# Kernel tuning notes

Hardware: AMD Instinct MI355X
Metric: run time of the kernel (lower is better)

Reference implementation:

```python
import jax, jax.numpy as jnp
import numpy as np

B, T, E, H, V = 64, 512, 512, 1024, 32000


def setup_inputs() -> dict:
    key = jax.random.key(0)
    k1, k2, k3, k4, k5 = jax.random.split(key, 5)
    scale = 1.0 / np.sqrt(H)
    return {
        "source": jax.random.randint(k1, (B, T), 0, V),
        "emb_table": jax.random.normal(k2, (V, E), dtype=jnp.float32),
        "W_ih": jax.random.normal(k3, (E, 4 * H), dtype=jnp.float32) * scale,
        "W_hh": jax.random.normal(k4, (H, 4 * H), dtype=jnp.float32) * scale,
        "b": jax.random.normal(k5, (4 * H,), dtype=jnp.float32) * scale,
    }


def reference(source, emb_table, W_ih, W_hh, b):
    # Embedding lookup: [B, T, E]
    embedded = emb_table[source]
    batch = source.shape[0]
    hidden = W_hh.shape[0]
    h0 = jnp.zeros((batch, hidden), dtype=emb_table.dtype)
    c0 = jnp.zeros((batch, hidden), dtype=emb_table.dtype)

    # Sequential LSTM cell loop over timesteps, expressed as lax.scan.
    xs = jnp.swapaxes(embedded, 0, 1)  # [T, B, E]

    def step(carry, x_t):
        h, c = carry
        z = x_t @ W_ih + h @ W_hh + b  # [B, 4H]
        i, f, g, o = jnp.split(z, 4, axis=-1)
        i = jax.nn.sigmoid(i)
        f = jax.nn.sigmoid(f)
        g = jnp.tanh(g)
        o = jax.nn.sigmoid(o)
        c_new = f * c + i * g
        h_new = o * jnp.tanh(c_new)
        return (h_new, c_new), None

    (h_T, c_T), _ = jax.lax.scan(step, (h0, c0), xs)
    return h_T, c_T
```

## Files before the change

### kernel.cpp

```cpp
#include <hip/hip_runtime.h>
#include <hip/hip_bf16.h>

#define TT 512
#define BB 64
#define EE 512
#define HH 1024

typedef __attribute__((ext_vector_type(8))) short short8;
typedef __attribute__((ext_vector_type(4))) float f32x4;
typedef __attribute__((ext_vector_type(4))) unsigned int u32x4;

#define WS_X     0
#define WS_WT    33554432
#define WS_HBUF  46137344
#define WS_PROBE 48496640

#define POISON 0x7F7F7F7Fu

static __device__ __forceinline__ unsigned short f2bf(float x) {
    unsigned int u = __float_as_uint(x);
    unsigned int r = (u + 0x7fffu + ((u >> 16) & 1u)) >> 16;
    return (unsigned short)r;
}

__global__ void embed_k(const int* __restrict__ src, const float* __restrict__ emb,
                        unsigned short* __restrict__ X) {
    int idx  = blockIdx.x * 256 + threadIdx.x;
    int base = idx * 4;
    int t = base >> 15;
    int r = base & 32767;
    int b = r >> 9;
    int e = r & 511;
    int v = src[b * TT + t];
    float4 f = *(const float4*)(emb + (size_t)v * EE + e);
    ushort4 s;
    s.x = f2bf(f.x); s.y = f2bf(f.y); s.z = f2bf(f.z); s.w = f2bf(f.w);
    *(ushort4*)(X + base) = s;
}

__global__ void wprep_k(const float* __restrict__ Wih, const float* __restrict__ Whh,
                        unsigned short* __restrict__ Wt, int* __restrict__ probe) {
    const int bid = blockIdx.x;
    const int kk  = bid % 48;
    const int ct  = bid / 48;
    const int tid = threadIdx.x;

    if (bid == 0 && tid == 0) {
        int xcd;
        asm volatile("s_getreg_b32 %0, hwreg(HW_REG_XCC_ID)" : "=s"(xcd));
        int* pr = probe;
        asm volatile("global_store_dword %0, %1, off sc0"
                     :: "v"(pr), "v"(xcd) : "memory");
        int v;
        asm volatile("global_load_dword %0, %1, off sc0\n\ts_waitcnt vmcnt(0)"
                     : "=v"(v) : "v"(pr) : "memory");
        pr[1] = v;
    }

    const int k0 = kk * 32, c0 = ct * 16;
    __shared__ float tile[32][17];
    for (int e = tid; e < 512; e += 256) {
        int kr = e >> 4, cc = e & 15;
        int k = k0 + kr;
        float v = (k < EE) ? Wih[(size_t)k * 4096 + c0 + cc]
                           : Whh[(size_t)(k - EE) * 4096 + c0 + cc];
        tile[kr][cc] = v;
    }
    __syncthreads();
    for (int e = tid; e < 512; e += 256) {
        int lane = e >> 3, j = e & 7;
        float v = tile[(lane >> 4) * 8 + j][lane & 15];
        Wt[(size_t)bid * 512 + e] = f2bf(v);
    }
}

__global__ __launch_bounds__(256, 1) void lstm_k(
    const unsigned short* __restrict__ X,
    const unsigned short* __restrict__ Wt,
    const float* __restrict__ bias,
    unsigned short* __restrict__ hbuf,
    float* __restrict__ out)
{
    const int g        = blockIdx.x;
    const int cg       = g & 63;
    const int rg       = g >> 6;
    const int row_base = rg * 16;
    const int ubase    = cg * 16;
    const int tid  = threadIdx.x;
    const int wave = tid >> 6;
    const int lane = tid & 63;
    const int lrow = lane & 15;
    const int quad = lane >> 4;
    const int erow = tid >> 4, eu = tid & 15;

    __shared__ float zred[2][4][4][16][17];

    const float bi_ = bias[          ubase + eu];
    const float bf_ = bias[HH      + ubase + eu];
    const float bg_ = bias[2 * HH  + ubase + eu];
    const float bo_ = bias[3 * HH  + ubase + eu];

    short8 wr[12][4];
#pragma unroll
    for (int i = 0; i < 12; ++i) {
        const int kk = i * 4 + wave;
#pragma unroll
        for (int g4 = 0; g4 < 4; ++g4) {
            const int ct = g4 * 64 + cg;
            wr[i][g4] = *(const short8*)(Wt + ((size_t)(ct * 48 + kk)) * 512 + lane * 8);
        }
    }

    float creg = 0.f;

    for (int t = 0; t < TT; ++t) {
        const unsigned short* xp = X + ((size_t)(t * BB) + row_base + lrow) * EE + quad * 8;
        short8 ax[4];
#pragma unroll
        for (int i = 0; i < 4; ++i)
            asm volatile("global_load_dwordx4 %0, %1, off"
                         : "=v"(ax[i]) : "v"(xp + (i * 4 + wave) * 32) : "memory");

        const unsigned short* hrow = hbuf
            + ((size_t)((t + 3) & 3) * BB + row_base + lrow) * HH + quad * 8;
        short8 ah[8];
        while (true) {
#pragma unroll
            for (int i = 0; i < 8; ++i)
                asm volatile("global_load_dwordx4 %0, %1, off sc1"
                             : "=v"(ah[i])
                             : "v"(hrow + (size_t)((i * 4 + wave) * 32)) : "memory");
            asm volatile("s_waitcnt vmcnt(0)" ::: "memory");
            __builtin_amdgcn_sched_barrier(0);
            int bad = 0;
#pragma unroll
            for (int i = 0; i < 8; ++i) {
                union { short8 v; unsigned int d[4]; } u; u.v = ah[i];
                bad |= (u.d[0] == POISON) | (u.d[1] == POISON)
                     | (u.d[2] == POISON) | (u.d[3] == POISON);
            }
            if (__all(bad == 0)) break;
        }
        __builtin_amdgcn_sched_barrier(0);

        f32x4 acc0 = {0.f,0.f,0.f,0.f}, acc1 = {0.f,0.f,0.f,0.f};
        f32x4 acc2 = {0.f,0.f,0.f,0.f}, acc3 = {0.f,0.f,0.f,0.f};

#pragma unroll
        for (int i = 0; i < 4; ++i) {
            acc0 = __builtin_amdgcn_mfma_f32_16x16x32_bf16(ax[i], wr[i][0], acc0, 0, 0, 0);
            acc1 = __builtin_amdgcn_mfma_f32_16x16x32_bf16(ax[i], wr[i][1], acc1, 0, 0, 0);
            acc2 = __builtin_amdgcn_mfma_f32_16x16x32_bf16(ax[i], wr[i][2], acc2, 0, 0, 0);
            acc3 = __builtin_amdgcn_mfma_f32_16x16x32_bf16(ax[i], wr[i][3], acc3, 0, 0, 0);
        }

#pragma unroll
        for (int i = 0; i < 8; ++i) {
            acc0 = __builtin_amdgcn_mfma_f32_16x16x32_bf16(ah[i], wr[i + 4][0], acc0, 0, 0, 0);
            acc1 = __builtin_amdgcn_mfma_f32_16x16x32_bf16(ah[i], wr[i + 4][1], acc1, 0, 0, 0);
            acc2 = __builtin_amdgcn_mfma_f32_16x16x32_bf16(ah[i], wr[i + 4][2], acc2, 0, 0, 0);
            acc3 = __builtin_amdgcn_mfma_f32_16x16x32_bf16(ah[i], wr[i + 4][3], acc3, 0, 0, 0);
        }

        if (lane < 8) {
            unsigned short* pp = hbuf
                + ((size_t)((t + 2) & 3) * BB + row_base + wave * 4 + (lane >> 1)) * HH
                + ubase + (lane & 1) * 8;
            u32x4 pz; pz.x = POISON; pz.y = POISON; pz.z = POISON; pz.w = POISON;
            asm volatile("global_store_dwordx4 %0, %1, off sc1"
                         :: "v"(pp), "v"(pz) : "memory");
        }

        const int zb = t & 1;
#pragma unroll
        for (int r = 0; r < 4; ++r) {
            zred[zb][wave][0][quad * 4 + r][lrow] = acc0[r];
            zred[zb][wave][1][quad * 4 + r][lrow] = acc1[r];
            zred[zb][wave][2][quad * 4 + r][lrow] = acc2[r];
            zred[zb][wave][3][quad * 4 + r][lrow] = acc3[r];
        }
        asm volatile("s_waitcnt lgkmcnt(0)" ::: "memory");
        asm volatile("s_barrier" ::: "memory");

        float zi = zred[zb][0][0][erow][eu] + zred[zb][1][0][erow][eu]
                 + zred[zb][2][0][erow][eu] + zred[zb][3][0][erow][eu] + bi_;
        float zf = zred[zb][0][1][erow][eu] + zred[zb][1][1][erow][eu]
                 + zred[zb][2][1][erow][eu] + zred[zb][3][1][erow][eu] + bf_;
        float zg = zred[zb][0][2][erow][eu] + zred[zb][1][2][erow][eu]
                 + zred[zb][2][2][erow][eu] + zred[zb][3][2][erow][eu] + bg_;
        float zo = zred[zb][0][3][erow][eu] + zred[zb][1][3][erow][eu]
                 + zred[zb][2][3][erow][eu] + zred[zb][3][3][erow][eu] + bo_;
        float iv = 1.f / (1.f + __expf(-zi));
        float fv = 1.f / (1.f + __expf(-zf));
        float gv = 1.f - 2.f / (__expf(2.f * zg) + 1.f);
        float ov = 1.f / (1.f + __expf(-zo));
        float c  = fv * creg + iv * gv;
        creg = c;
        float th = 1.f - 2.f / (__expf(2.f * c) + 1.f);
        float h  = ov * th;

        if (t < TT - 1) {
            float hp1 = __shfl_xor(h, 1);
            unsigned int v01 = (unsigned int)f2bf(h) | ((unsigned int)f2bf(hp1) << 16);
            unsigned int v23 = (unsigned int)__shfl_xor((int)v01, 2);
            unsigned int v45 = (unsigned int)__shfl_xor((int)v01, 4);
            unsigned int v67 = (unsigned int)__shfl_xor((int)v23, 4);
            if ((eu & 7) == 0) {
                u32x4 pk; pk.x = v01; pk.y = v23; pk.z = v45; pk.w = v67;
                unsigned short* hw = hbuf + ((size_t)(t & 3) * BB + row_base + erow) * HH
                                   + ubase + eu;
                asm volatile("global_store_dwordx4 %0, %1, off sc1"
                             :: "v"(hw), "v"(pk) : "memory");
            }
        } else {
            out[(row_base + erow) * HH + ubase + eu] = h;
            out[BB * HH + (row_base + erow) * HH + ubase + eu] = c;
        }
    }
}

extern "C" void kernel_launch(void* const* d_in, const int* in_sizes, int n_in,
                              void* d_out, int out_size, void* d_ws, size_t ws_size,
                              hipStream_t stream) {
    const int*   src  = (const int*)d_in[0];
    const float* emb  = (const float*)d_in[1];
    const float* Wih  = (const float*)d_in[2];
    const float* Whh  = (const float*)d_in[3];
    const float* bias = (const float*)d_in[4];
    float* out = (float*)d_out;

    char* ws = (char*)d_ws;
    unsigned short* X     = (unsigned short*)(ws + WS_X);
    unsigned short* Wt    = (unsigned short*)(ws + WS_WT);
    unsigned short* hbuf  = (unsigned short*)(ws + WS_HBUF);
    int*            probe = (int*)(ws + WS_PROBE);

    hipMemsetAsync(hbuf, 0x7F, (size_t)4 * BB * HH * 2, stream);
    hipMemsetAsync((char*)hbuf + (size_t)3 * BB * HH * 2, 0, (size_t)BB * HH * 2, stream);
    embed_k<<<dim3(16384), dim3(256), 0, stream>>>(src, emb, X);
    wprep_k<<<dim3(12288), dim3(256), 0, stream>>>(Wih, Whh, Wt, probe);
    lstm_k<<<dim3(256), dim3(256), 0, stream>>>(X, Wt, bias, hbuf, out);
}
```

Baseline: 1.998 ms.

## Replace poison-flag handshake with per-word timestep tags in hidden-state buffer

The hidden-state exchange buffer now stores each bf16 value in a 32-bit word whose upper half holds the timestep tag. Consumers spin until every loaded word carries the expected tag, then pack the low halves into bf16 MFMA operands. This drops the separate poison store to the buffer two steps ahead and the cross-lane shuffle packing before the store, which shortens the producer side of each recurrence step. The cost is twice the load traffic per step on the latency-critical h read, plus narrower 4-byte stores from every thread.

```diff
diff --git a/kernel.cpp b/kernel.cpp
--- a/kernel.cpp
+++ b/kernel.cpp
@@ -5,6 +5,7 @@
 #define BB 64
 #define EE 512
 #define HH 1024
+#define HB (BB * HH)
 
 typedef __attribute__((ext_vector_type(8))) short short8;
 typedef __attribute__((ext_vector_type(4))) float f32x4;
@@ -14,8 +15,6 @@
 #define WS_WT    33554432
 #define WS_HBUF  46137344
 #define WS_PROBE 48496640
-
-#define POISON 0x7F7F7F7Fu
 
 static __device__ __forceinline__ unsigned short f2bf(float x) {
     unsigned int u = __float_as_uint(x);
@@ -78,7 +77,7 @@
     const unsigned short* __restrict__ X,
     const unsigned short* __restrict__ Wt,
     const float* __restrict__ bias,
-    unsigned short* __restrict__ hbuf,
+    unsigned int* __restrict__ hbuf,
     float* __restrict__ out)
 {
     const int g        = blockIdx.x;
@@ -121,27 +120,45 @@
             asm volatile("global_load_dwordx4 %0, %1, off"
                          : "=v"(ax[i]) : "v"(xp + (i * 4 + wave) * 32) : "memory");
 
-        const unsigned short* hrow = hbuf
-            + ((size_t)((t + 3) & 3) * BB + row_base + lrow) * HH + quad * 8;
+        const unsigned int* hb = hbuf + ((size_t)((t + 3) & 3)) * HB
+                               + (size_t)(row_base + lrow) * HH + 32 * wave + quad * 8;
+        u32x4 hv[16];
+        {
+            const unsigned int tg = (unsigned int)t;
+            while (true) {
+#pragma unroll
+                for (int i = 0; i < 8; ++i) {
+                    const unsigned int* p = hb + 128 * i;
+                    asm volatile("global_load_dwordx4 %0, %1, off sc1"
+                                 : "=v"(hv[2 * i]) : "v"(p) : "memory");
+                    asm volatile("global_load_dwordx4 %0, %1, off sc1"
+                                 : "=v"(hv[2 * i + 1]) : "v"(p + 4) : "memory");
+                }
+                asm volatile("s_waitcnt vmcnt(0)" ::: "memory");
+                __builtin_amdgcn_sched_barrier(0);
+                unsigned int bad = 0;
+#pragma unroll
+                for (int k = 0; k < 16; ++k) {
+                    bad |= (hv[k].x >> 16) ^ tg;
+                    bad |= (hv[k].y >> 16) ^ tg;
+                    bad |= (hv[k].z >> 16) ^ tg;
+                    bad |= (hv[k].w >> 16) ^ tg;
+                }
+                if (__all(bad == 0)) break;
+            }
+            __builtin_amdgcn_sched_barrier(0);
+        }
+
         short8 ah[8];
-        while (true) {
-#pragma unroll
-            for (int i = 0; i < 8; ++i)
-                asm volatile("global_load_dwordx4 %0, %1, off sc1"
-                             : "=v"(ah[i])
-                             : "v"(hrow + (size_t)((i * 4 + wave) * 32)) : "memory");
-            asm volatile("s_waitcnt vmcnt(0)" ::: "memory");
-            __builtin_amdgcn_sched_barrier(0);
-            int bad = 0;
-#pragma unroll
-            for (int i = 0; i < 8; ++i) {
-                union { short8 v; unsigned int d[4]; } u; u.v = ah[i];
-                bad |= (u.d[0] == POISON) | (u.d[1] == POISON)
-                     | (u.d[2] == POISON) | (u.d[3] == POISON);
-            }
-            if (__all(bad == 0)) break;
-        }
-        __builtin_amdgcn_sched_barrier(0);
+#pragma unroll
+        for (int i = 0; i < 8; ++i) {
+            union { unsigned int u[4]; short8 v; } pk;
+            pk.u[0] = (hv[2 * i].x & 0xFFFFu)     | (hv[2 * i].y << 16);
+            pk.u[1] = (hv[2 * i].z & 0xFFFFu)     | (hv[2 * i].w << 16);
+            pk.u[2] = (hv[2 * i + 1].x & 0xFFFFu) | (hv[2 * i + 1].y << 16);
+            pk.u[3] = (hv[2 * i + 1].z & 0xFFFFu) | (hv[2 * i + 1].w << 16);
+            ah[i] = pk.v;
+        }
 
         f32x4 acc0 = {0.f,0.f,0.f,0.f}, acc1 = {0.f,0.f,0.f,0.f};
         f32x4 acc2 = {0.f,0.f,0.f,0.f}, acc3 = {0.f,0.f,0.f,0.f};
@@ -160,15 +177,6 @@
             acc1 = __builtin_amdgcn_mfma_f32_16x16x32_bf16(ah[i], wr[i + 4][1], acc1, 0, 0, 0);
             acc2 = __builtin_amdgcn_mfma_f32_16x16x32_bf16(ah[i], wr[i + 4][2], acc2, 0, 0, 0);
             acc3 = __builtin_amdgcn_mfma_f32_16x16x32_bf16(ah[i], wr[i + 4][3], acc3, 0, 0, 0);
-        }
-
-        if (lane < 8) {
-            unsigned short* pp = hbuf
-                + ((size_t)((t + 2) & 3) * BB + row_base + wave * 4 + (lane >> 1)) * HH
-                + ubase + (lane & 1) * 8;
-            u32x4 pz; pz.x = POISON; pz.y = POISON; pz.z = POISON; pz.w = POISON;
-            asm volatile("global_store_dwordx4 %0, %1, off sc1"
-                         :: "v"(pp), "v"(pz) : "memory");
         }
 
         const int zb = t & 1;
@@ -200,18 +208,12 @@
         float h  = ov * th;
 
         if (t < TT - 1) {
-            float hp1 = __shfl_xor(h, 1);
-            unsigned int v01 = (unsigned int)f2bf(h) | ((unsigned int)f2bf(hp1) << 16);
-            unsigned int v23 = (unsigned int)__shfl_xor((int)v01, 2);
-            unsigned int v45 = (unsigned int)__shfl_xor((int)v01, 4);
-            unsigned int v67 = (unsigned int)__shfl_xor((int)v23, 4);
-            if ((eu & 7) == 0) {
-                u32x4 pk; pk.x = v01; pk.y = v23; pk.z = v45; pk.w = v67;
-                unsigned short* hw = hbuf + ((size_t)(t & 3) * BB + row_base + erow) * HH
-                                   + ubase + eu;
-                asm volatile("global_store_dwordx4 %0, %1, off sc1"
-                             :: "v"(hw), "v"(pk) : "memory");
-            }
+            unsigned int wv = (unsigned int)f2bf(h)
+                            | (((unsigned int)(t + 1) & 0xFFFFu) << 16);
+            unsigned int* hw = hbuf + (size_t)(t & 3) * HB
+                             + (size_t)(row_base + erow) * HH + ubase + eu;
+            asm volatile("global_store_dword %0, %1, off sc1"
+                         :: "v"(hw), "v"(wv) : "memory");
         } else {
             out[(row_base + erow) * HH + ubase + eu] = h;
             out[BB * HH + (row_base + erow) * HH + ubase + eu] = c;
@@ -232,11 +234,10 @@
     char* ws = (char*)d_ws;
     unsigned short* X     = (unsigned short*)(ws + WS_X);
     unsigned short* Wt    = (unsigned short*)(ws + WS_WT);
-    unsigned short* hbuf  = (unsigned short*)(ws + WS_HBUF);
+    unsigned int*   hbuf  = (unsigned int*)(ws + WS_HBUF);
     int*            probe = (int*)(ws + WS_PROBE);
 
-    hipMemsetAsync(hbuf, 0x7F, (size_t)4 * BB * HH * 2, stream);
-    hipMemsetAsync((char*)hbuf + (size_t)3 * BB * HH * 2, 0, (size_t)BB * HH * 2, stream);
+    hipMemsetAsync(hbuf, 0, (size_t)4 * HB * 4, stream);
     embed_k<<<dim3(16384), dim3(256), 0, stream>>>(src, emb, X);
     wprep_k<<<dim3(12288), dim3(256), 0, stream>>>(Wih, Whh, Wt, probe);
     lstm_k<<<dim3(256), dim3(256), 0, stream>>>(X, Wt, bias, hbuf, out);
```

Result: slower. 2.760 ms (+38.2%).
